# Performance work log

Hardware: AMD Instinct MI355X
Metric: run time of the kernel (lower is better)

## Reference

```python
import jax, jax.numpy as jnp
import numpy as np

# Cleaned/faithful JAX port of TATLMPLayer. The original torch code has obvious
# typos (edge_type_feature_embedding used before assignment, self.weight_mlp vs
# self._weight_mlp, missing dim= in concatenate, elementwise mult of (B,E,K) with
# (K,D)); we implement the clearly intended math: two-level masked-softmax
# message passing over an incidence matrix H, gumbel-softmax typed edge
# embeddings, and a 4-head cross-attention to polyline features.

NEG_SLOPE = 0.01  # torch leaky_relu default
TAU = 0.5         # gumbel-softmax temperature 1/2


def _mlp(x, W1, b1, W2, b2):
    return jnp.maximum(x @ W1 + b1, 0.0) @ W2 + b2


def setup_inputs() -> dict:
    B, N, E, P, D, T, K, Hd = 2, 256, 512, 256, 128, 8, 8, 256
    key = jax.random.key(0)
    ks = jax.random.split(key, 40)
    g = lambda i, shape, s=0.05: jax.random.normal(ks[i], shape, dtype=jnp.float32) * s
    return {
        "agent_features": jax.random.normal(ks[0], (B, N, D), dtype=jnp.float32),
        "agent_types": jax.random.uniform(ks[1], (B, N, T), dtype=jnp.float32),
        "polyline_features": jax.random.normal(ks[2], (B, P, D), dtype=jnp.float32),
        "H": (jax.random.uniform(ks[3], (B, E, N)) < 0.1).astype(jnp.float32),
        "type_emb": g(4, (K, D)),
        "w_W1": g(5, (2 * D, Hd)), "w_b1": g(6, (Hd,)), "w_W2": g(7, (Hd, 1)), "w_b2": g(8, (1,)),
        "d_W1": g(9, (D + T, Hd)), "d_b1": g(10, (Hd,)), "d_W2": g(11, (Hd, K)), "d_b2": g(12, (K,)),
        "f_W1": g(13, (D + T, Hd)), "f_b1": g(14, (Hd,)), "f_W2": g(15, (Hd, 1)), "f_b2": g(16, (1,)),
        "o_W1": g(17, (4 * D, Hd)), "o_b1": g(18, (Hd,)), "o_W2": g(19, (Hd, D)), "o_b2": g(20, (D,)),
        "q_W": g(21, (3 * D, D)), "q_b": g(22, (D,)),
        "k_W": g(23, (D, D)), "k_b": g(24, (D,)),
        "v_W": g(25, (D, D)), "v_b": g(26, (D,)),
        "iq_W": g(27, (D, D)), "iq_b": g(28, (D,)),
        "ik_W": g(29, (D, D)), "ik_b": g(30, (D,)),
        "iv_W": g(31, (D, D)), "iv_b": g(32, (D,)),
        "op_W": g(33, (D, D)), "op_b": g(34, (D,)),
    }


def reference(agent_features, agent_types, polyline_features, H, type_emb,
              w_W1, w_b1, w_W2, w_b2, d_W1, d_b1, d_W2, d_b2,
              f_W1, f_b1, f_W2, f_b2, o_W1, o_b1, o_W2, o_b2,
              q_W, q_b, k_W, k_b, v_W, v_b,
              iq_W, iq_b, ik_W, ik_b, iv_W, iv_b, op_W, op_b):
    B, N, D = agent_features.shape
    E = H.shape[1]

    # level 1: incidence-aggregated edge features
    ef_init = jnp.einsum('ben,bnd->bed', H, agent_features)            # (B,E,D)
    pair = jnp.concatenate([
        jnp.broadcast_to(ef_init[:, :, None, :], (B, E, N, D)),
        jnp.broadcast_to(agent_features[:, None, :, :], (B, E, N, D))], axis=-1)
    ew = _mlp(pair, w_W1, w_b1, w_W2, w_b2)[..., 0]                    # (B,E,N)
    Hw = jax.nn.softmax(ew * H, axis=2) * H
    edge_features = jnp.einsum('ben,bnd->bed', Hw, agent_features)     # (B,E,D)

    # typed edge embedding via gumbel-softmax over edge types
    edge_type = jnp.einsum('ben,bnt->bet', H, agent_types)             # (B,E,T)
    et = jnp.concatenate([edge_features, edge_type], axis=-1)          # (B,E,D+T)
    logits = _mlp(et, d_W1, d_b1, d_W2, d_b2)                          # (B,E,K)
    u = jax.random.uniform(jax.random.key(42), logits.shape, minval=1e-6, maxval=1.0 - 1e-6)
    gumbel = -jnp.log(-jnp.log(u))
    distribution = jax.nn.softmax((logits + gumbel) / TAU, axis=-1)
    factor = jax.nn.sigmoid(_mlp(et, f_W1, f_b1, f_W2, f_b2))          # (B,E,1)
    edge_type_embedding = jnp.einsum('bek,kd->bed', factor * distribution, type_emb)

    # level 2: masked edge->agent message passing
    pair2 = jnp.concatenate([
        jnp.broadcast_to(edge_type_embedding[:, :, None, :], (B, E, N, D)),
        jnp.broadcast_to(agent_features[:, None, :, :], (B, E, N, D))], axis=-1)
    pair2 = pair2 * H[..., None]
    hw2 = jnp.where(_mlp(pair2, w_W1, w_b1, w_W2, w_b2)[..., 0] > 0,
                    _mlp(pair2, w_W1, w_b1, w_W2, w_b2)[..., 0], 0.0)
    # leaky relu (single-eval form)
    raw2 = _mlp(pair2, w_W1, w_b1, w_W2, w_b2)[..., 0]
    hw2 = jnp.where(raw2 > 0, raw2, NEG_SLOPE * raw2)                  # (B,E,N)
    Hw2 = jax.nn.softmax(hw2, axis=2) * H
    msg = jnp.einsum('ben,bef->bnf', Hw2,
                     jnp.concatenate([edge_features, edge_type_embedding], axis=-1))
    agent_feat = jnp.concatenate([msg, agent_features], axis=-1)       # (B,N,3D)

    # cross-attention to polylines (4 heads)
    Q = agent_feat @ q_W + q_b
    Kp = polyline_features @ k_W + k_b
    Vp = polyline_features @ v_W + v_b
    q2 = Q @ iq_W + iq_b
    k2 = Kp @ ik_W + ik_b
    v2 = Vp @ iv_W + iv_b
    nh, hd = 4, D // 4
    qh = q2.reshape(B, N, nh, hd)
    kh = k2.reshape(B, -1, nh, hd)
    vh = v2.reshape(B, -1, nh, hd)
    att = jax.nn.softmax(jnp.einsum('bqhd,bkhd->bhqk', qh, kh) / jnp.sqrt(jnp.float32(hd)), axis=-1)
    o = jnp.einsum('bhqk,bkhd->bqhd', att, vh).reshape(B, N, D)
    polyline_new = o @ op_W + op_b                                     # (B,N,D)

    agent_new = _mlp(jnp.concatenate([agent_feat, polyline_new], axis=-1),
                     o_W1, o_b1, o_W2, o_b2)                           # (B,N,D)
    return agent_new, polyline_new
```

## Files before the change

kernel.cpp:

```cpp
#include <hip/hip_runtime.h>
#include <math.h>

#define BB 2
#define NN 256
#define EE 512
#define PP 256
#define DD 128
#define TT 8
#define KK 8
#define HDIM 256

#define WS_G      0
#define WS_C0     8192
#define WS_EF0    8256
#define WS_ETYPE  139328
#define WS_V      147520
#define WS_EDGEF  278592
#define WS_ETE    409664
#define WS_HWT    540736
#define WS_AGF    802880
#define WS_Q2     999488
#define WS_K2     1065024
#define WS_V2     1130560

#define GB_INC  16
#define GB_V    1040
#define GB_KV   1168
#define GB_END  1296

__device__ inline unsigned rotl32(unsigned x, int d){ return (x<<d)|(x>>(32-d)); }

__device__ inline float bits_to_gumbel(unsigned bits){
  float f = __uint_as_float((bits>>9)|0x3f800000u) - 1.0f;
  const float minv = 1e-6f;
  const float maxv = 1.0f - 1e-6f;
  float u = f*(maxv-minv) + minv;
  u = fmaxf(minv, u);
  return -logf(-logf(u));
}

__device__ __forceinline__ void f4fma(float4& a, float x, const float4& w){
  a.x += x*w.x; a.y += x*w.y; a.z += x*w.z; a.w += x*w.w;
}
// ... 74 lines not shown
  #pragma unroll
  for (int r=0;r<4;r++) *(float4*)&part[(ks*4+r)*DD+c]=a[r];
  __syncthreads();
  int cc=t&127, rh=t>>7;
  for (int rr=rh; rr<4; rr+=2){
    float s=0.f;
    #pragma unroll
    for (int k2=0;k2<8;k2++) s+=part[(k2*4+rr)*DD+cc];
    dst[(size_t)(r0+rr)*DD+cc]=s+bias[cc];
  }
  __syncthreads();
}

__global__ void prep_kernel(float* g, float* c0, const float* w_b1,
                            const float* w_W2, const float* w_b2,
                            const float* Hm, const float* af, const float* at,
                            float* ef0, float* etype,
                            const float* wW1, float* Vout,
                            const float* pf,
                            const float* kW, const float* kb, const float* ikW, const float* ikb,
                            const float* vW, const float* vb, const float* ivW, const float* ivb,
                            float* k2, float* v2){
  __shared__ int   ecomp[NN];
  __shared__ int   wcnt[4];
  __shared__ float accl[2][DD];
  __shared__ float acctl[2][TT];
  __shared__ float xs[4][DD];
  __shared__ float part[4*4*HDIM];
  __shared__ float wred[16];
  __shared__ float bufB[4][DD];
  int blk = blockIdx.x;
  int t = threadIdx.x;
  int lane = t & 63, wid = t >> 6;

  if (blk < GB_INC){
    int j = blk*256 + t;
    {
      const unsigned k0=0u, k1=42u;
      const unsigned ks2 = k0^k1^0x1BD11BDAu;
      unsigned x0 = (unsigned)j, x1 = (unsigned)j + 4096u;
      const int r0[4]={13,15,26,6}, r1[4]={17,29,16,24};
      x0 += k0; x1 += k1;
      #pragma unroll
      for(int i=0;i<4;i++){ x0+=x1; x1=rotl32(x1,r0[i]); x1^=x0; }
      x0+=k1; x1+=ks2+1u;
      #pragma unroll
      for(int i=0;i<4;i++){ x0+=x1; x1=rotl32(x1,r1[i]); x1^=x0; }
      x0+=ks2; x1+=k0+2u;
      #pragma unroll
      for(int i=0;i<4;i++){ x0+=x1; x1=rotl32(x1,r0[i]); x1^=x0; }
      x0+=k0; x1+=k1+3u;
      #pragma unroll
      for(int i=0;i<4;i++){ x0+=x1; x1=rotl32(x1,r1[i]); x1^=x0; }
      x0+=k1; x1+=ks2+4u;
      #pragma unroll
      for(int i=0;i<4;i++){ x0+=x1; x1=rotl32(x1,r0[i]); x1^=x0; }
      x0+=ks2; x1+=k0+5u;
      g[j]      = bits_to_gumbel(x0);
      g[j+4096] = bits_to_gumbel(x1);
    }
    if (blk == 0){
      float v4[4];
      v4[0] = fmaxf(w_b1[t],0.f)*w_W2[t]; v4[1]=0.f; v4[2]=0.f; v4[3]=0.f;
      block_reduce4_sum(v4, wred);
      if (t==0) c0[0] = v4[0] + w_b2[0];
    }
  } else if (blk < GB_V){
    int be = blk - GB_INC;
    int b  = be >> 9;
    const float* Hrow = Hm + (size_t)be*NN;
    int n = t;
    bool pred = (Hrow[n] != 0.f);
    unsigned long long mask = __ballot(pred);
    if (lane==0) wcnt[wid] = __popcll(mask);
    int off = __popcll(mask & ((1ull<<lane)-1ull));
    __syncthreads();
    int wb = 0;
    for (int ww=0; ww<wid; ww++) wb += wcnt[ww];
    if (pred) ecomp[wb+off] = n;
    int total = wcnt[0]+wcnt[1]+wcnt[2]+wcnt[3];
    __syncthreads();
    int d = t & 127, h2 = t >> 7;
    float acc = 0.f, acct = 0.f;
    for (int i=h2; i<total; i+=2){
      int n2 = ecomp[i];
      acc += af[((size_t)b*NN+n2)*DD + d];
      if (d < TT) acct += at[((size_t)b*NN+n2)*TT + d];
    }
    accl[h2][d] = acc;
    if (d < TT) acctl[h2][d] = acct;
    __syncthreads();
    if (t < DD) ef0[(size_t)be*DD + t] = accl[0][t] + accl[1][t];
    if (t < TT) etype[(size_t)be*TT + t] = acctl[0][t] + acctl[1][t];
  } else if (blk < GB_KV){
    int r0 = (blk - GB_V)*4;
    const float* W = wW1 + (size_t)DD*HDIM;
    for (int i=t;i<4*DD;i+=256) xs[i>>7][i&127] = af[(size_t)(r0+(i>>7))*DD + (i&127)];
    __syncthreads();
    int c = (t&63)*4, ks = t>>6;
    float4 acc[4];
    #pragma unroll
    for (int r=0;r<4;r++) acc[r]=make_float4(0.f,0.f,0.f,0.f);
    #pragma unroll 8
    for (int i=ks*32; i<ks*32+32; i++){
      float4 w = *(const float4*)&W[(size_t)i*HDIM + c];
      #pragma unroll
      for (int r=0;r<4;r++) f4fma(acc[r], xs[r][i], w);
    }
    #pragma unroll
    for (int r=0;r<4;r++) *(float4*)&part[(ks*4+r)*HDIM + c] = acc[r];
    __syncthreads();
    #pragma unroll
    for (int r=0;r<4;r++){
      float s = (part[(0*4+r)*HDIM+t] + part[(1*4+r)*HDIM+t])
              + (part[(2*4+r)*HDIM+t] + part[(3*4+r)*HDIM+t]);
      Vout[(size_t)(r0+r)*HDIM + t] = s;
    }
  } else {
    int r0 = (blk - GB_KV)*4;
    for (int i=t;i<4*DD;i+=256) xs[i>>7][i&127] = pf[(size_t)(r0+(i>>7))*DD + (i&127)];
    __syncthreads();
    mlp128_lds (xs, kW, kb, bufB, part, t);
    mlp128_glob(bufB, ikW, ikb, k2, r0, part, t);
    mlp128_lds (xs, vW, vb, bufB, part, t);
    mlp128_glob(bufB, ivW, ivb, v2, r0, part, t);
  }
}

__global__ void l1_fused_kernel(const float* ef0, const float* Vm, const float* Hm,
                                const float* af, const float* wW1, const float* wb1,
                                const float* wW2, const float* wb2, float* edgef){
  __shared__ float xs[4][DD];
  __shared__ float part[4*4*HDIM];
  __shared__ float u[4][HDIM];
  __shared__ float w2l[HDIM];
  __shared__ float hwls[4][NN];
  __shared__ float wred[16];
  __shared__ int   ncomp[4][NN];
  __shared__ float ncw[4][NN];
  __shared__ int   ncnt[4];
  int e0 = blockIdx.x*4;
  int b  = e0 >> 9;
  int t  = threadIdx.x;
  int lane = t & 63, wid = t >> 6;

  for (int i=t;i<4*DD;i+=256) xs[i>>7][i&127] = ef0[(size_t)(e0+(i>>7))*DD + (i&127)];
  w2l[t] = wW2[t];
  __syncthreads();
  {
    int c = (t&63)*4, ks = t>>6;
    float4 acc[4];
    #pragma unroll
    for (int r=0;r<4;r++) acc[r]=make_float4(0.f,0.f,0.f,0.f);
    #pragma unroll 8
    for (int i=ks*32; i<ks*32+32; i++){
      float4 w = *(const float4*)&wW1[(size_t)i*HDIM + c];
      #pragma unroll
      for (int r=0;r<4;r++) f4fma(acc[r], xs[r][i], w);
    }
    #pragma unroll
    for (int r=0;r<4;r++) *(float4*)&part[(ks*4+r)*HDIM + c] = acc[r];
  }
  __syncthreads();
  {
    float bv = wb1[t];
    #pragma unroll
    for (int r=0;r<4;r++){
      float s = (part[(0*4+r)*HDIM+t] + part[(1*4+r)*HDIM+t])
              + (part[(2*4+r)*HDIM+t] + part[(3*4+r)*HDIM+t]);
      u[r][t] = s + bv;
    }
  }
  __syncthreads();
  int n = t;
  const float4* Vrow = (const float4*)(Vm + ((size_t)(b*NN)+n)*HDIM);
  float acc[4]={0.f,0.f,0.f,0.f};
  #pragma unroll 4
  for (int ii=0;ii<HDIM/4;ii++){
    float4 v = Vrow[ii];
    float w0=w2l[4*ii+0], w1=w2l[4*ii+1], wc=w2l[4*ii+2], w3=w2l[4*ii+3];
    #pragma unroll
    for (int r=0;r<4;r++){
      acc[r] += fmaxf(u[r][4*ii+0]+v.x,0.f)*w0
              + fmaxf(u[r][4*ii+1]+v.y,0.f)*w1
              + fmaxf(u[r][4*ii+2]+v.z,0.f)*wc
              + fmaxf(u[r][4*ii+3]+v.w,0.f)*w3;
    }
  }
  float b2v = wb2[0];
  float x[4], hv[4];
  #pragma unroll
  for (int r=0;r<4;r++){
    hv[r] = Hm[(size_t)(e0+r)*NN + n];
    x[r] = (hv[r]!=0.f) ? (acc[r]+b2v) : 0.f;
  }
  float m4[4]={x[0],x[1],x[2],x[3]};
  block_reduce4_max(m4, wred);
  float p4[4];
  #pragma unroll
  for (int r=0;r<4;r++) p4[r]=expf(x[r]-m4[r]);
  float s4[4]={p4[0],p4[1],p4[2],p4[3]};
  block_reduce4_sum(s4, wred);
  #pragma unroll
  for (int r=0;r<4;r++)
    hwls[r][n] = (hv[r]!=0.f) ? p4[r]/s4[r] : 0.f;
  __syncthreads();
  {
    int r = wid;
    int base = 0;
    #pragma unroll
    for (int c4=0;c4<4;c4++){
      int n2 = c4*64 + lane;
      float w = hwls[r][n2];
      bool pred = (w != 0.f);
      unsigned long long mask = __ballot(pred);
      int off = __popcll(mask & ((1ull<<lane)-1ull));
      if (pred){ ncomp[r][base+off] = n2; ncw[r][base+off] = w; }
      base += __popcll(mask);
    }
    if (lane==0) ncnt[r] = base;
  }
  __syncthreads();
  {
    int d = t & 127, eh = t >> 7;
    #pragma unroll
    for (int rr=0;rr<2;rr++){
      int r = eh*2 + rr;
      int tot = ncnt[r];
      float a = 0.f;
      for (int i=0;i<tot;i++)
        a += ncw[r][i]*af[((size_t)b*NN+ncomp[r][i])*DD + d];
      edgef[(size_t)(e0+r)*DD + d] = a;
    }
  }
}

__global__ void l2_fused_kernel(const float* edgef, const float* etype, const float* g,
                                const float* dW1, const float* db1, const float* dW2, const float* db2,
                                const float* fW1, const float* fb1, const float* fW2, const float* fb2,
                                const float* type_emb,
                                const float* wW1, const float* wb1, const float* wW2, const float* wb2,
                                const float* c0p, const float* Hm, const float* Vm,
                                float* ete_g, float* HwT){
  __shared__ float et4[4][DD+TT+8];
  __shared__ float partD[4*4*HDIM];
  __shared__ float partF[4*4*HDIM];
  __shared__ float hd4[4][HDIM];
  __shared__ float w2s[HDIM*KK];
  __shared__ float redsm[256];
  __shared__ float wred[16];
  __shared__ float facs[4];
  __shared__ float zz[4][KK];
  __shared__ float pzs[4][KK];
  __shared__ float fdv[4][KK];
  int e0 = blockIdx.x*4;
  int b  = e0 >> 9;
  int t  = threadIdx.x;
  const int KW = DD+TT;

  for (int i=t;i<4*KW;i+=256){
    int r=i/KW, cc=i%KW;
    et4[r][cc] = (cc<DD) ? edgef[(size_t)(e0+r)*DD+cc] : etype[(size_t)(e0+r)*TT + (cc-DD)];
  }
  for (int i=t;i<HDIM*KK;i+=256) w2s[i] = dW2[i];
  __syncthreads();
  int c=(t&63)*4, ks=t>>6;
  {
    float4 ad4[4], af4[4];
    #pragma unroll
    for (int r=0;r<4;r++){ ad4[r]=make_float4(0.f,0.f,0.f,0.f); af4[r]=make_float4(0.f,0.f,0.f,0.f); }
    #pragma unroll 4
    for (int i=ks*34;i<ks*34+34;i++){
      float4 wd = *(const float4*)&dW1[(size_t)i*HDIM+c];
      float4 wf = *(const float4*)&fW1[(size_t)i*HDIM+c];
      #pragma unroll
      for (int r=0;r<4;r++){ float x=et4[r][i]; f4fma(ad4[r],x,wd); f4fma(af4[r],x,wf); }
    }
    #pragma unroll
    for (int r=0;r<4;r++){
      *(float4*)&partD[(ks*4+r)*HDIM+c]=ad4[r];
      *(float4*)&partF[(ks*4+r)*HDIM+c]=af4[r];
    }
  }
  __syncthreads();
  {
    float bd = db1[t];
    float bf = fb1[t], fw = fW2[t];
    float v4[4];
    #pragma unroll
    for (int r=0;r<4;r++){
      float sd = (partD[(0*4+r)*HDIM+t]+partD[(1*4+r)*HDIM+t])
               + (partD[(2*4+r)*HDIM+t]+partD[(3*4+r)*HDIM+t]);
      hd4[r][t] = fmaxf(sd+bd, 0.f);
      float sf = (partF[(0*4+r)*HDIM+t]+partF[(1*4+r)*HDIM+t])
               + (partF[(2*4+r)*HDIM+t]+partF[(3*4+r)*HDIM+t]);
      v4[r] = fmaxf(sf+bf,0.f)*fw;
    }
    block_reduce4_sum(v4, wred);
    if (t<4) facs[t] = 1.f/(1.f+expf(-(v4[t]+fb2[0])));
  }
  {
    int rr_ = t>>6, kk_ = (t>>3)&7, jj_ = t&7;
    float lp = 0.f;
    #pragma unroll 4
    for (int i=0;i<32;i++){
      int h = jj_ + 8*i;
      lp += hd4[rr_][h]*w2s[h*KK + kk_];
    }
    redsm[t] = lp;
  }
// ... 21 lines not shown
    for (int k2=0;k2<KK;k2++) s += pzs[r][k2];
    fdv[r][k] = facs[r]*pzs[r][k]/s;
  }
  __syncthreads();
  {
    int d = t&127;
    #pragma unroll
    for (int rr=0;rr<2;rr++){
      int r = 2*rr + (t>>7);
      float a = 0.f;
      #pragma unroll
      for (int k=0;k<KK;k++) a += fdv[r][k]*type_emb[(size_t)k*DD + d];
      et4[r][d] = a;
      ete_g[(size_t)(e0+r)*DD + d] = a;
    }
    w2s[t] = wW2[t];
  }
  __syncthreads();
  {
    float4 a[4];
    #pragma unroll
    for (int r=0;r<4;r++) a[r]=make_float4(0.f,0.f,0.f,0.f);
    #pragma unroll 8
    for (int i=ks*32;i<ks*32+32;i++){
      float4 w = *(const float4*)&wW1[(size_t)i*HDIM+c];
      #pragma unroll
      for (int r=0;r<4;r++) f4fma(a[r], et4[r][i], w);
    }
    #pragma unroll
    for (int r=0;r<4;r++) *(float4*)&partD[(ks*4+r)*HDIM+c]=a[r];
  }
  __syncthreads();
  {
    float bv = wb1[t];
    #pragma unroll
    for (int r=0;r<4;r++){
      float s = (partD[(0*4+r)*HDIM+t]+partD[(1*4+r)*HDIM+t])
              + (partD[(2*4+r)*HDIM+t]+partD[(3*4+r)*HDIM+t]);
      hd4[r][t] = s + bv;
    }
  }
  __syncthreads();
  {
    int n = t;
    const float4* Vrow = (const float4*)(Vm + ((size_t)(b*NN)+n)*HDIM);
    float acc[4]={0.f,0.f,0.f,0.f};
    #pragma unroll 4
    for (int ii=0;ii<HDIM/4;ii++){
      float4 v = Vrow[ii];
      float w0=w2s[4*ii+0], w1=w2s[4*ii+1], wc=w2s[4*ii+2], w3=w2s[4*ii+3];
      #pragma unroll
      for (int r=0;r<4;r++){
        acc[r] += fmaxf(hd4[r][4*ii+0]+v.x,0.f)*w0
                + fmaxf(hd4[r][4*ii+1]+v.y,0.f)*w1
                + fmaxf(hd4[r][4*ii+2]+v.z,0.f)*wc
                + fmaxf(hd4[r][4*ii+3]+v.w,0.f)*w3;
      }
    }
    float b2v = wb2[0];
    float c0 = c0p[0];
    float x[4], hv[4];
    #pragma unroll
    for (int r=0;r<4;r++){
      hv[r] = Hm[(size_t)(e0+r)*NN + n];
      float raw = (hv[r]!=0.f) ? (acc[r]+b2v) : c0;
// ... 4 lines not shown
    float p4[4];
    #pragma unroll
    for (int r=0;r<4;r++) p4[r]=expf(x[r]-m4[r]);
    float s4[4]={p4[0],p4[1],p4[2],p4[3]};
    block_reduce4_sum(s4, wred);
    int eb = e0 & 511;
    float4 o4;
    o4.x = (hv[0]!=0.f)? p4[0]/s4[0] : 0.f;
    o4.y = (hv[1]!=0.f)? p4[1]/s4[1] : 0.f;
    o4.z = (hv[2]!=0.f)? p4[2]/s4[2] : 0.f;
    o4.w = (hv[3]!=0.f)? p4[3]/s4[3] : 0.f;
    *(float4*)(HwT + ((size_t)(b*NN)+n)*EE + eb) = o4;
  }
}

__global__ void msgq2_kernel(const float* HwT, const float* edgef, const float* ete,
                             const float* af, const float* qW, const float* qb,
                             const float* iqW, const float* iqb,
                             float* agf, float* q2){
  __shared__ int   ecomp[EE];
  __shared__ float wcomp[EE];
  __shared__ int   wcnt[4];
  __shared__ float agfl[3*DD];
  __shared__ float part[8*DD];
  __shared__ float Qs[DD];
  int bn = blockIdx.x; int b = bn>>8; int f = threadIdx.x;
  int lane = f & 63, wid = f >> 6;
  const float* wrow = HwT + (size_t)bn*EE;
  int total = 0;
  #pragma unroll
  for (int p=0;p<2;p++){
    int e = p*256 + f;
    float w = wrow[e];
    bool pred = (w != 0.f);
    unsigned long long mask = __ballot(pred);
    if (lane==0) wcnt[wid] = __popcll(mask);
    int off = __popcll(mask & ((1ull<<lane)-1ull));
    __syncthreads();
    int wb = total;
    for (int ww=0; ww<wid; ww++) wb += wcnt[ww];
    if (pred){ ecomp[wb+off] = e; wcomp[wb+off] = w; }
    total += wcnt[0]+wcnt[1]+wcnt[2]+wcnt[3];
    __syncthreads();
  }
  float acc = 0.f;
  const float* srcbase = (f < DD) ? (edgef + (size_t)b*EE*DD + f)
                                  : (ete   + (size_t)b*EE*DD + (f-DD));
  for (int i=0;i<total;i++){
    acc += wcomp[i] * srcbase[(size_t)ecomp[i]*DD];
  }
  agfl[f] = acc;
  agf[(size_t)bn*(3*DD)+f] = acc;
  if (f < DD){
    float av = af[(size_t)bn*DD + f];
    agfl[2*DD+f] = av;
    agf[(size_t)bn*(3*DD) + 2*DD + f] = av;
  }
  __syncthreads();
  int c=(f&31)*4, ks=f>>5;
  {
    float4 a = make_float4(0.f,0.f,0.f,0.f);
    #pragma unroll 4
    for (int i=ks*48;i<ks*48+48;i++){
      float4 w = *(const float4*)&qW[(size_t)i*DD+c];
      f4fma(a, agfl[i], w);
    }
    *(float4*)&part[ks*DD+c]=a;
  }
  __syncthreads();
  if (f<DD){
    float s=0.f;
    #pragma unroll
    for (int k=0;k<8;k++) s+=part[k*DD+f];
    Qs[f]=s+qb[f];
  }
  __syncthreads();
  {
    float4 a = make_float4(0.f,0.f,0.f,0.f);
    #pragma unroll 4
    for (int i=ks*16;i<ks*16+16;i++){
      float4 w = *(const float4*)&iqW[(size_t)i*DD+c];
      f4fma(a, Qs[i], w);
    }
    *(float4*)&part[ks*DD+c]=a;
  }
  __syncthreads();
  if (f<DD){
    float s=0.f;
    #pragma unroll
    for (int k=0;k<8;k++) s+=part[k*DD+f];
    q2[(size_t)bn*DD+f]=s+iqb[f];
  }
}

__global__ void attnfinal_kernel(const float* q2, const float* k2, const float* v2,
                                 const float* op_W, const float* op_b,
                                 const float* agf,
                                 const float* oW1, const float* ob1,
                                 const float* oW2, const float* ob2,
                                 float* pnew, float* anew){
  __shared__ float qr[2][DD];
  __shared__ float att[2][4][PP+1];
  __shared__ float o_l[2][DD];
  __shared__ float part[8*2*DD];
  __shared__ float pnl[2][DD];
  __shared__ float xs[2][4*DD];
  __shared__ float hid[2][HDIM];
  int r0 = blockIdx.x*2; int b = r0 >> 8; int t = threadIdx.x;
  for (int i=t;i<2*DD;i+=256) qr[i>>7][i&127] = q2[(size_t)(r0+(i>>7))*DD + (i&127)];
  __syncthreads();
  const float scale = 0.17677669529663687f;
  const float* krow = k2 + ((size_t)(b*PP) + t)*DD;
  #pragma unroll
  for (int h=0;h<4;h++){
    const float4* k4 = (const float4*)(krow + h*32);
    float s[2]={0.f,0.f};
    #pragma unroll
    for (int jj=0;jj<8;jj++){
      float4 kk = k4[jj];
      #pragma unroll
      for (int r=0;r<2;r++){
        s[r] += qr[r][h*32+jj*4+0]*kk.x + qr[r][h*32+jj*4+1]*kk.y
              + qr[r][h*32+jj*4+2]*kk.z + qr[r][h*32+jj*4+3]*kk.w;
      }
    }
    #pragma unroll
    for (int r=0;r<2;r++) att[r][h][t] = s[r]*scale;
  }
  __syncthreads();
  {
    int lane = t & 63, wid = t >> 6;
    for (int q = wid; q < 8; q += 4){
      int r = q >> 2, h = q & 3;
      float v0 = att[r][h][lane],     v1 = att[r][h][lane+64],
            ve = att[r][h][lane+128], v3 = att[r][h][lane+192];
      float m = fmaxf(fmaxf(v0,v1), fmaxf(ve,v3));
      #pragma unroll
      for (int s2=32;s2>0;s2>>=1) m = fmaxf(m, __shfl_xor(m, s2, 64));
      float e0 = expf(v0-m), e1 = expf(v1-m), e2 = expf(ve-m), e3 = expf(v3-m);
      float ss = (e0+e1)+(e2+e3);
      #pragma unroll
      for (int s2=32;s2>0;s2>>=1) ss += __shfl_xor(ss, s2, 64);
      float inv = 1.f/ss;
      att[r][h][lane] = e0*inv; att[r][h][lane+64] = e1*inv;
      att[r][h][lane+128] = e2*inv; att[r][h][lane+192] = e3*inv;
    }
  }
  __syncthreads();
  int c=(t&31)*4, ps=t>>5; int h2 = c>>5;
  {
    float4 acc[2];
    #pragma unroll
    for (int r=0;r<2;r++) acc[r]=make_float4(0.f,0.f,0.f,0.f);
    #pragma unroll 4
    for (int i=0;i<32;i++){
      int p = ps*32+i;
      float4 v = *(const float4*)&v2[((size_t)(b*PP)+p)*DD + c];
      #pragma unroll
      for (int r=0;r<2;r++) f4fma(acc[r], att[r][h2][p], v);
    }
    #pragma unroll
    for (int r=0;r<2;r++) *(float4*)&part[(ps*2+r)*DD+c]=acc[r];
  }
  __syncthreads();
  {
    int cc=t&127, r=t>>7;
    float s=0.f;
    #pragma unroll
    for (int k2_=0;k2_<8;k2_++) s+=part[(k2_*2+r)*DD+cc];
    o_l[r][cc]=s;
  }
  __syncthreads();
  {
    float4 a2[2];
    #pragma unroll
    for (int r=0;r<2;r++) a2[r]=make_float4(0.f,0.f,0.f,0.f);
    #pragma unroll 4
    for (int i=ps*16;i<ps*16+16;i++){
      float4 w = *(const float4*)&op_W[(size_t)i*DD + c];
      #pragma unroll
      for (int r=0;r<2;r++) f4fma(a2[r], o_l[r][i], w);
    }
    #pragma unroll
    for (int r=0;r<2;r++) *(float4*)&part[(ps*2+r)*DD+c]=a2[r];
  }
  __syncthreads();
  {
    int cc=t&127, r=t>>7;
    float s=0.f;
    #pragma unroll
    for (int k2_=0;k2_<8;k2_++) s+=part[(k2_*2+r)*DD+cc];
    float pv = s+op_b[cc];
    pnl[r][cc] = pv;
    pnew[(size_t)(r0+r)*DD+cc] = pv;
  }
  for (int i=t;i<2*(3*DD);i+=256){
    int r = i/(3*DD), cc = i%(3*DD);
    xs[r][cc] = agf[(size_t)(r0+r)*(3*DD)+cc];
  }
  __syncthreads();
  if (t < 2*DD){
    int r = t>>7, cc = t&127;
    xs[r][3*DD+cc] = pnl[r][cc];
  }
  __syncthreads();
  {
    int c1=(t&63)*4, ks1=t>>6;
    float4 acc[2];
    #pragma unroll
    for (int r=0;r<2;r++) acc[r]=make_float4(0.f,0.f,0.f,0.f);
    #pragma unroll 8
    for (int i=ks1*128;i<ks1*128+128;i++){
      float4 w = *(const float4*)&oW1[(size_t)i*HDIM+c1];
      #pragma unroll
      for (int r=0;r<2;r++) f4fma(acc[r], xs[r][i], w);
    }
    #pragma unroll
    for (int r=0;r<2;r++) *(float4*)&part[(ks1*2+r)*HDIM+c1]=acc[r];
  }
  __syncthreads();
  {
    float bv = ob1[t];
    #pragma unroll
    for (int r=0;r<2;r++){
      float s = (part[(0*2+r)*HDIM+t]+part[(1*2+r)*HDIM+t])
              + (part[(2*2+r)*HDIM+t]+part[(3*2+r)*HDIM+t]);
      hid[r][t] = fmaxf(s+bv, 0.f);
    }
  }
  __syncthreads();
// ... 3 lines not shown
    for (int r=0;r<2;r++) a2[r]=make_float4(0.f,0.f,0.f,0.f);
    #pragma unroll 8
    for (int h=ps*32;h<ps*32+32;h++){
      float4 w = *(const float4*)&oW2[(size_t)h*DD+c];
      #pragma unroll
      for (int r=0;r<2;r++) f4fma(a2[r], hid[r][h], w);
    }
    #pragma unroll
    for (int r=0;r<2;r++) *(float4*)&part[(ps*2+r)*DD+c]=a2[r];
  }
  __syncthreads();
  {
    int cc=t&127, r=t>>7;
    float s=0.f;
    #pragma unroll
    for (int k2_=0;k2_<8;k2_++) s+=part[(k2_*2+r)*DD+cc];
    anew[(size_t)(r0+r)*DD+cc]=s+ob2[cc];
  }
}

extern "C" void kernel_launch(void* const* d_in, const int* in_sizes, int n_in,
                              void* d_out, int out_size, void* d_ws, size_t ws_size,
                              hipStream_t stream) {
  const float* af       = (const float*)d_in[0];
  const float* at       = (const float*)d_in[1];
  const float* pf       = (const float*)d_in[2];
  const float* Hm       = (const float*)d_in[3];
  const float* type_emb = (const float*)d_in[4];
  const float* w_W1 = (const float*)d_in[5];
  const float* w_b1 = (const float*)d_in[6];
  const float* w_W2 = (const float*)d_in[7];
  const float* w_b2 = (const float*)d_in[8];
// ... 17 lines not shown
  const float* v_b  = (const float*)d_in[26];
  const float* iq_W = (const float*)d_in[27];
  const float* iq_b = (const float*)d_in[28];
  const float* ik_W = (const float*)d_in[29];
  const float* ik_b = (const float*)d_in[30];
  const float* iv_W = (const float*)d_in[31];
  const float* iv_b = (const float*)d_in[32];
  const float* op_W = (const float*)d_in[33];
  const float* op_b = (const float*)d_in[34];

  float* ws   = (float*)d_ws;
  float* out  = (float*)d_out;
  float* anew = out;
  float* pnew = out + BB*NN*DD;

  prep_kernel<<<GB_END, 256, 0, stream>>>(
      ws+WS_G, ws+WS_C0, w_b1, w_W2, w_b2,
      Hm, af, at, ws+WS_EF0, ws+WS_ETYPE, w_W1, ws+WS_V,
      pf, k_W,k_b,ik_W,ik_b, v_W,v_b,iv_W,iv_b,
      ws+WS_K2, ws+WS_V2);
  l1_fused_kernel<<<256,256,0,stream>>>(
      ws+WS_EF0, ws+WS_V, Hm, af, w_W1, w_b1, w_W2, w_b2, ws+WS_EDGEF);
  l2_fused_kernel<<<256,256,0,stream>>>(
      ws+WS_EDGEF, ws+WS_ETYPE, ws+WS_G,
      d_W1,d_b1,d_W2,d_b2, f_W1,f_b1,f_W2,f_b2, type_emb,
      w_W1, w_b1, w_W2, w_b2, ws+WS_C0, Hm, ws+WS_V,
      ws+WS_ETE, ws+WS_HWT);
  msgq2_kernel<<<BB*NN,256,0,stream>>>(
      ws+WS_HWT, ws+WS_EDGEF, ws+WS_ETE, af,
      q_W, q_b, iq_W, iq_b, ws+WS_AGF, ws+WS_Q2);
  attnfinal_kernel<<<256,256,0,stream>>>(
      ws+WS_Q2, ws+WS_K2, ws+WS_V2, op_W, op_b,
      ws+WS_AGF, o_W1,o_b1,o_W2,o_b2, pnew, anew);
}
```

Measured before the change: 91.78 us.

## Fuse edge stages into one kernel and merge message/Q with attention kernel

The incidence-gather that produced ef0/etype moves out of the prep kernel and into a single edge kernel, which now also runs the level-1 softmax and the level-2 typed-edge stage, so ef0, etype and the intermediate edge features no longer round-trip through global memory. The message aggregation and Q projection are merged into the attention/output kernel, which processes two agents per block and drops the agf and q2 workspace buffers. This cuts five launches to three and removes several global writes and reads. In exchange, the fused kernels are longer and serialised, with large LDS footprints that can lower occupancy. The agent kernel runs only 256 blocks, each doing the per-agent gather twice in sequence.

Result: no change. 93.58 us (+2.0%).

```diff
diff --git a/kernel.cpp b/kernel.cpp
--- a/kernel.cpp
+++ b/kernel.cpp
@@ -12,21 +12,16 @@
 
 #define WS_G      0
 #define WS_C0     8192
-#define WS_EF0    8256
-#define WS_ETYPE  139328
-#define WS_V      147520
-#define WS_EDGEF  278592
-#define WS_ETE    409664
-#define WS_HWT    540736
-#define WS_AGF    802880
-#define WS_Q2     999488
-#define WS_K2     1065024
-#define WS_V2     1130560
-
-#define GB_INC  16
-#define GB_V    1040
-#define GB_KV   1168
-#define GB_END  1296
+#define WS_V      8256
+#define WS_EDGEF  139328
+#define WS_ETE    270400
+#define WS_HWT    401472
+#define WS_K2     663616
+#define WS_V2     729152
+
+#define PB_GUM 16
+#define PB_V   144
+#define PB_END 272
 
 __device__ inline unsigned rotl32(unsigned x, int d){ return (x<<d)|(x>>(32-d)); }
 
@@ -131,47 +126,40 @@
 
 __global__ void prep_kernel(float* g, float* c0, const float* w_b1,
                             const float* w_W2, const float* w_b2,
-                            const float* Hm, const float* af, const float* at,
-                            float* ef0, float* etype,
-                            const float* wW1, float* Vout,
+                            const float* af, const float* wW1, float* Vout,
                             const float* pf,
                             const float* kW, const float* kb, const float* ikW, const float* ikb,
                             const float* vW, const float* vb, const float* ivW, const float* ivb,
                             float* k2, float* v2){
-  __shared__ int   ecomp[NN];
-  __shared__ int   wcnt[4];
-  __shared__ float accl[2][DD];
-  __shared__ float acctl[2][TT];
   __shared__ float xs[4][DD];
   __shared__ float part[4*4*HDIM];
   __shared__ float wred[16];
   __shared__ float bufB[4][DD];
   int blk = blockIdx.x;
   int t = threadIdx.x;
-  int lane = t & 63, wid = t >> 6;
-
-  if (blk < GB_INC){
+
+  if (blk < PB_GUM){
     int j = blk*256 + t;
     {
       const unsigned k0=0u, k1=42u;
       const unsigned ks2 = k0^k1^0x1BD11BDAu;
       unsigned x0 = (unsigned)j, x1 = (unsigned)j + 4096u;
-      const int r0[4]={13,15,26,6}, r1[4]={17,29,16,24};
+      const int r0_[4]={13,15,26,6}, r1_[4]={17,29,16,24};
       x0 += k0; x1 += k1;
       #pragma unroll
-      for(int i=0;i<4;i++){ x0+=x1; x1=rotl32(x1,r0[i]); x1^=x0; }
+      for(int i=0;i<4;i++){ x0+=x1; x1=rotl32(x1,r0_[i]); x1^=x0; }
       x0+=k1; x1+=ks2+1u;
       #pragma unroll
-      for(int i=0;i<4;i++){ x0+=x1; x1=rotl32(x1,r1[i]); x1^=x0; }
+      for(int i=0;i<4;i++){ x0+=x1; x1=rotl32(x1,r1_[i]); x1^=x0; }
       x0+=ks2; x1+=k0+2u;
       #pragma unroll
-      for(int i=0;i<4;i++){ x0+=x1; x1=rotl32(x1,r0[i]); x1^=x0; }
+      for(int i=0;i<4;i++){ x0+=x1; x1=rotl32(x1,r0_[i]); x1^=x0; }
       x0+=k0; x1+=k1+3u;
       #pragma unroll
-      for(int i=0;i<4;i++){ x0+=x1; x1=rotl32(x1,r1[i]); x1^=x0; }
+      for(int i=0;i<4;i++){ x0+=x1; x1=rotl32(x1,r1_[i]); x1^=x0; }
       x0+=k1; x1+=ks2+4u;
       #pragma unroll
-      for(int i=0;i<4;i++){ x0+=x1; x1=rotl32(x1,r0[i]); x1^=x0; }
+      for(int i=0;i<4;i++){ x0+=x1; x1=rotl32(x1,r0_[i]); x1^=x0; }
       x0+=ks2; x1+=k0+5u;
       g[j]      = bits_to_gumbel(x0);
       g[j+4096] = bits_to_gumbel(x1);
@@ -182,35 +170,8 @@
       block_reduce4_sum(v4, wred);
       if (t==0) c0[0] = v4[0] + w_b2[0];
     }
-  } else if (blk < GB_V){
-    int be = blk - GB_INC;
-    int b  = be >> 9;
-    const float* Hrow = Hm + (size_t)be*NN;
-    int n = t;
-    bool pred = (Hrow[n] != 0.f);
-    unsigned long long mask = __ballot(pred);
-    if (lane==0) wcnt[wid] = __popcll(mask);
-    int off = __popcll(mask & ((1ull<<lane)-1ull));
-    __syncthreads();
-    int wb = 0;
-    for (int ww=0; ww<wid; ww++) wb += wcnt[ww];
-    if (pred) ecomp[wb+off] = n;
-    int total = wcnt[0]+wcnt[1]+wcnt[2]+wcnt[3];
-    __syncthreads();
-    int d = t & 127, h2 = t >> 7;
-    float acc = 0.f, acct = 0.f;
-    for (int i=h2; i<total; i+=2){
-      int n2 = ecomp[i];
-      acc += af[((size_t)b*NN+n2)*DD + d];
-      if (d < TT) acct += at[((size_t)b*NN+n2)*TT + d];
-    }
-    accl[h2][d] = acc;
-    if (d < TT) acctl[h2][d] = acct;
-    __syncthreads();
-    if (t < DD) ef0[(size_t)be*DD + t] = accl[0][t] + accl[1][t];
-    if (t < TT) etype[(size_t)be*TT + t] = acctl[0][t] + acctl[1][t];
-  } else if (blk < GB_KV){
-    int r0 = (blk - GB_V)*4;
+  } else if (blk < PB_V){
+    int r0 = (blk - PB_GUM)*4;
     const float* W = wW1 + (size_t)DD*HDIM;
     for (int i=t;i<4*DD;i+=256) xs[i>>7][i&127] = af[(size_t)(r0+(i>>7))*DD + (i&127)];
     __syncthreads();
@@ -234,7 +195,7 @@
       Vout[(size_t)(r0+r)*HDIM + t] = s;
     }
   } else {
-    int r0 = (blk - GB_KV)*4;
+    int r0 = (blk - PB_V)*4;
     for (int i=t;i<4*DD;i+=256) xs[i>>7][i&127] = pf[(size_t)(r0+(i>>7))*DD + (i&127)];
     __syncthreads();
     mlp128_lds (xs, kW, kb, bufB, part, t);
@@ -244,145 +205,155 @@
   }
 }
 
-__global__ void l1_fused_kernel(const float* ef0, const float* Vm, const float* Hm,
-                                const float* af, const float* wW1, const float* wb1,
-                                const float* wW2, const float* wb2, float* edgef){
-  __shared__ float xs[4][DD];
-  __shared__ float part[4*4*HDIM];
-  __shared__ float u[4][HDIM];
+__global__ void edge_kernel(const float* Hm, const float* af, const float* at,
+                            const float* Vm,
+                            const float* wW1, const float* wb1, const float* wW2, const float* wb2,
+                            const float* dW1, const float* db1, const float* dW2, const float* db2,
+                            const float* fW1, const float* fb1, const float* fW2, const float* fb2,
+                            const float* type_emb, const float* g, const float* c0p,
+                            float* edgef_g, float* ete_g, float* HwT){
+  __shared__ float bufA[4*4*HDIM];
+  __shared__ float bufB[4*4*HDIM];
+  __shared__ float w2s[HDIM*KK];
   __shared__ float w2l[HDIM];
-  __shared__ float hwls[4][NN];
-  __shared__ float wred[16];
-  __shared__ int   ncomp[4][NN];
-  __shared__ float ncw[4][NN];
-  __shared__ int   ncnt[4];
-  int e0 = blockIdx.x*4;
-  int b  = e0 >> 9;
-  int t  = threadIdx.x;
-  int lane = t & 63, wid = t >> 6;
-
-  for (int i=t;i<4*DD;i+=256) xs[i>>7][i&127] = ef0[(size_t)(e0+(i>>7))*DD + (i&127)];
-  w2l[t] = wW2[t];
-  __syncthreads();
-  {
-    int c = (t&63)*4, ks = t>>6;
-    float4 acc[4];
-    #pragma unroll
-    for (int r=0;r<4;r++) acc[r]=make_float4(0.f,0.f,0.f,0.f);
-    #pragma unroll 8
-    for (int i=ks*32; i<ks*32+32; i++){
-      float4 w = *(const float4*)&wW1[(size_t)i*HDIM + c];
-      #pragma unroll
-      for (int r=0;r<4;r++) f4fma(acc[r], xs[r][i], w);
-    }
-    #pragma unroll
-    for (int r=0;r<4;r++) *(float4*)&part[(ks*4+r)*HDIM + c] = acc[r];
-  }
-  __syncthreads();
-  {
-    float bv = wb1[t];
-    #pragma unroll
-    for (int r=0;r<4;r++){
-      float s = (part[(0*4+r)*HDIM+t] + part[(1*4+r)*HDIM+t])
-              + (part[(2*4+r)*HDIM+t] + part[(3*4+r)*HDIM+t]);
-      u[r][t] = s + bv;
-    }
-  }
-  __syncthreads();
-  int n = t;
-  const float4* Vrow = (const float4*)(Vm + ((size_t)(b*NN)+n)*HDIM);
-  float acc[4]={0.f,0.f,0.f,0.f};
-  #pragma unroll 4
-  for (int ii=0;ii<HDIM/4;ii++){
-    float4 v = Vrow[ii];
-    float w0=w2l[4*ii+0], w1=w2l[4*ii+1], wc=w2l[4*ii+2], w3=w2l[4*ii+3];
-    #pragma unroll
-    for (int r=0;r<4;r++){
-      acc[r] += fmaxf(u[r][4*ii+0]+v.x,0.f)*w0
-              + fmaxf(u[r][4*ii+1]+v.y,0.f)*w1
-              + fmaxf(u[r][4*ii+2]+v.z,0.f)*wc
-              + fmaxf(u[r][4*ii+3]+v.w,0.f)*w3;
-    }
-  }
-  float b2v = wb2[0];
-  float x[4], hv[4];
-  #pragma unroll
-  for (int r=0;r<4;r++){
-    hv[r] = Hm[(size_t)(e0+r)*NN + n];
-    x[r] = (hv[r]!=0.f) ? (acc[r]+b2v) : 0.f;
-  }
-  float m4[4]={x[0],x[1],x[2],x[3]};
-  block_reduce4_max(m4, wred);
-  float p4[4];
-  #pragma unroll
-  for (int r=0;r<4;r++) p4[r]=expf(x[r]-m4[r]);
-  float s4[4]={p4[0],p4[1],p4[2],p4[3]};
-  block_reduce4_sum(s4, wred);
-  #pragma unroll
-  for (int r=0;r<4;r++)
-    hwls[r][n] = (hv[r]!=0.f) ? p4[r]/s4[r] : 0.f;
-  __syncthreads();
-  {
-    int r = wid;
-    int base = 0;
-    #pragma unroll
-    for (int c4=0;c4<4;c4++){
-      int n2 = c4*64 + lane;
-      float w = hwls[r][n2];
-      bool pred = (w != 0.f);
-      unsigned long long mask = __ballot(pred);
-      int off = __popcll(mask & ((1ull<<lane)-1ull));
-      if (pred){ ncomp[r][base+off] = n2; ncw[r][base+off] = w; }
-      base += __popcll(mask);
-    }
-    if (lane==0) ncnt[r] = base;
-  }
-  __syncthreads();
-  {
-    int d = t & 127, eh = t >> 7;
-    #pragma unroll
-    for (int rr=0;rr<2;rr++){
-      int r = eh*2 + rr;
-      int tot = ncnt[r];
-      float a = 0.f;
-      for (int i=0;i<tot;i++)
-        a += ncw[r][i]*af[((size_t)b*NN+ncomp[r][i])*DD + d];
-      edgef[(size_t)(e0+r)*DD + d] = a;
-    }
-  }
-}
-
-__global__ void l2_fused_kernel(const float* edgef, const float* etype, const float* g,
-                                const float* dW1, const float* db1, const float* dW2, const float* db2,
-                                const float* fW1, const float* fb1, const float* fW2, const float* fb2,
-                                const float* type_emb,
-                                const float* wW1, const float* wb1, const float* wW2, const float* wb2,
-                                const float* c0p, const float* Hm, const float* Vm,
-                                float* ete_g, float* HwT){
-  __shared__ float et4[4][DD+TT+8];
-  __shared__ float partD[4*4*HDIM];
-  __shared__ float partF[4*4*HDIM];
+  __shared__ float et4[4][144];
   __shared__ float hd4[4][HDIM];
-  __shared__ float w2s[HDIM*KK];
   __shared__ float redsm[256];
   __shared__ float wred[16];
   __shared__ float facs[4];
   __shared__ float zz[4][KK];
   __shared__ float pzs[4][KK];
   __shared__ float fdv[4][KK];
+  __shared__ int   hcnt[4];
+  float* u    = bufB;
+  float* hwls = bufB + 1024;
+  int*   hcomp= (int*)(bufB + 2048);
+
   int e0 = blockIdx.x*4;
   int b  = e0 >> 9;
   int t  = threadIdx.x;
-  const int KW = DD+TT;
-
-  for (int i=t;i<4*KW;i+=256){
-    int r=i/KW, cc=i%KW;
-    et4[r][cc] = (cc<DD) ? edgef[(size_t)(e0+r)*DD+cc] : etype[(size_t)(e0+r)*TT + (cc-DD)];
-  }
+  int lane = t & 63, wid = t >> 6;
+
+  w2l[t] = wW2[t];
   for (int i=t;i<HDIM*KK;i+=256) w2s[i] = dW2[i];
-  __syncthreads();
-  int c=(t&63)*4, ks=t>>6;
-  {
+
+  {
+    int r = wid;
+    const float* Hrow = Hm + (size_t)(e0+r)*NN;
+    int base = 0;
+    #pragma unroll
+    for (int c4=0;c4<4;c4++){
+      int n2 = c4*64 + lane;
+      bool pred = (Hrow[n2] != 0.f);
+      unsigned long long mask = __ballot(pred);
+      int off = __popcll(mask & ((1ull<<lane)-1ull));
+      if (pred) hcomp[r*256+base+off] = n2;
+      base += __popcll(mask);
+    }
+    if (lane==0) hcnt[r] = base;
+  }
+  __syncthreads();
+  {
+    int d = t & 127, eh = t >> 7;
+    #pragma unroll
+    for (int rr=0;rr<2;rr++){
+      int r = eh*2 + rr;
+      int tot = hcnt[r];
+      float a = 0.f, a2 = 0.f;
+      for (int i=0;i<tot;i++){
+        int n2 = hcomp[r*256+i];
+        a += af[((size_t)b*NN+n2)*DD + d];
+        if (d < TT) a2 += at[((size_t)b*NN+n2)*TT + d];
+      }
+      et4[r][d] = a;
+      if (d < TT) et4[r][DD+d] = a2;
+    }
+  }
+  __syncthreads();
+  {
+    int c=(t&63)*4, ks=t>>6;
+    float4 acc[4];
+    #pragma unroll
+    for (int r=0;r<4;r++) acc[r]=make_float4(0.f,0.f,0.f,0.f);
+    #pragma unroll 8
+    for (int i=ks*32; i<ks*32+32; i++){
+      float4 w = *(const float4*)&wW1[(size_t)i*HDIM + c];
+      #pragma unroll
+      for (int r=0;r<4;r++) f4fma(acc[r], et4[r][i], w);
+    }
+    #pragma unroll
+    for (int r=0;r<4;r++) *(float4*)&bufA[(ks*4+r)*HDIM + c] = acc[r];
+  }
+  __syncthreads();
+  {
+    float bv = wb1[t];
+    #pragma unroll
+    for (int r=0;r<4;r++){
+      float s = (bufA[(0*4+r)*HDIM+t] + bufA[(1*4+r)*HDIM+t])
+              + (bufA[(2*4+r)*HDIM+t] + bufA[(3*4+r)*HDIM+t]);
+      u[r*HDIM + t] = s + bv;
+    }
+  }
+  __syncthreads();
+  {
+    int n = t;
+    const float4* Vrow = (const float4*)(Vm + ((size_t)(b*NN)+n)*HDIM);
+    float acc[4]={0.f,0.f,0.f,0.f};
+    #pragma unroll 4
+    for (int ii=0;ii<HDIM/4;ii++){
+      float4 v = Vrow[ii];
+      float w0=w2l[4*ii+0], w1=w2l[4*ii+1], wc=w2l[4*ii+2], w3=w2l[4*ii+3];
+      #pragma unroll
+      for (int r=0;r<4;r++){
+        acc[r] += fmaxf(u[r*HDIM+4*ii+0]+v.x,0.f)*w0
+                + fmaxf(u[r*HDIM+4*ii+1]+v.y,0.f)*w1
+                + fmaxf(u[r*HDIM+4*ii+2]+v.z,0.f)*wc
+                + fmaxf(u[r*HDIM+4*ii+3]+v.w,0.f)*w3;
+      }
+    }
+    float b2v = wb2[0];
+    float x[4], hv[4];
+    #pragma unroll
+    for (int r=0;r<4;r++){
+      hv[r] = Hm[(size_t)(e0+r)*NN + n];
+      x[r] = (hv[r]!=0.f) ? (acc[r]+b2v) : 0.f;
+    }
+    float m4[4]={x[0],x[1],x[2],x[3]};
+    block_reduce4_max(m4, wred);
+    float p4[4];
+    #pragma unroll
+    for (int r=0;r<4;r++) p4[r]=expf(x[r]-m4[r]);
+    float s4[4]={p4[0],p4[1],p4[2],p4[3]};
+    block_reduce4_sum(s4, wred);
+    #pragma unroll
+    for (int r=0;r<4;r++)
+      hwls[r*NN+n] = (hv[r]!=0.f) ? p4[r]/s4[r] : 0.f;
+  }
+  __syncthreads();
+  {
+    int d = t & 127, eh = t >> 7;
+    float eg[2];
+    #pragma unroll
+    for (int rr=0;rr<2;rr++){
+      int r = eh*2 + rr;
+      int tot = hcnt[r];
+      float a = 0.f;
+      for (int i=0;i<tot;i++){
+        int n2 = hcomp[r*256+i];
+        a += hwls[r*NN+n2]*af[((size_t)b*NN+n2)*DD + d];
+      }
+      eg[rr] = a;
+    }
+    #pragma unroll
+    for (int rr=0;rr<2;rr++){
+      int r = eh*2 + rr;
+      et4[r][d] = eg[rr];
+      edgef_g[(size_t)(e0+r)*DD + d] = eg[rr];
+    }
+  }
+  __syncthreads();
+  {
+    int c=(t&63)*4, ks=t>>6;
     float4 ad4[4], af4[4];
     #pragma unroll
     for (int r=0;r<4;r++){ ad4[r]=make_float4(0.f,0.f,0.f,0.f); af4[r]=make_float4(0.f,0.f,0.f,0.f); }
@@ -395,8 +366,8 @@
     }
     #pragma unroll
     for (int r=0;r<4;r++){
-      *(float4*)&partD[(ks*4+r)*HDIM+c]=ad4[r];
-      *(float4*)&partF[(ks*4+r)*HDIM+c]=af4[r];
+      *(float4*)&bufA[(ks*4+r)*HDIM+c]=ad4[r];
+      *(float4*)&bufB[(ks*4+r)*HDIM+c]=af4[r];
     }
   }
   __syncthreads();
@@ -406,11 +377,11 @@
     float v4[4];
     #pragma unroll
     for (int r=0;r<4;r++){
-      float sd = (partD[(0*4+r)*HDIM+t]+partD[(1*4+r)*HDIM+t])
-               + (partD[(2*4+r)*HDIM+t]+partD[(3*4+r)*HDIM+t]);
+      float sd = (bufA[(0*4+r)*HDIM+t]+bufA[(1*4+r)*HDIM+t])
+               + (bufA[(2*4+r)*HDIM+t]+bufA[(3*4+r)*HDIM+t]);
       hd4[r][t] = fmaxf(sd+bd, 0.f);
-      float sf = (partF[(0*4+r)*HDIM+t]+partF[(1*4+r)*HDIM+t])
-               + (partF[(2*4+r)*HDIM+t]+partF[(3*4+r)*HDIM+t]);
+      float sf = (bufB[(0*4+r)*HDIM+t]+bufB[(1*4+r)*HDIM+t])
+               + (bufB[(2*4+r)*HDIM+t]+bufB[(3*4+r)*HDIM+t]);
       v4[r] = fmaxf(sf+bf,0.f)*fw;
     }
     block_reduce4_sum(v4, wred);
@@ -462,10 +433,10 @@
       et4[r][d] = a;
       ete_g[(size_t)(e0+r)*DD + d] = a;
     }
-    w2s[t] = wW2[t];
-  }
-  __syncthreads();
-  {
+  }
+  __syncthreads();
+  {
+    int c=(t&63)*4, ks=t>>6;
     float4 a[4];
     #pragma unroll
     for (int r=0;r<4;r++) a[r]=make_float4(0.f,0.f,0.f,0.f);
@@ -476,15 +447,15 @@
       for (int r=0;r<4;r++) f4fma(a[r], et4[r][i], w);
     }
     #pragma unroll
-    for (int r=0;r<4;r++) *(float4*)&partD[(ks*4+r)*HDIM+c]=a[r];
+    for (int r=0;r<4;r++) *(float4*)&bufA[(ks*4+r)*HDIM+c]=a[r];
   }
   __syncthreads();
   {
     float bv = wb1[t];
     #pragma unroll
     for (int r=0;r<4;r++){
-      float s = (partD[(0*4+r)*HDIM+t]+partD[(1*4+r)*HDIM+t])
-              + (partD[(2*4+r)*HDIM+t]+partD[(3*4+r)*HDIM+t]);
+      float s = (bufA[(0*4+r)*HDIM+t]+bufA[(1*4+r)*HDIM+t])
+              + (bufA[(2*4+r)*HDIM+t]+bufA[(3*4+r)*HDIM+t]);
       hd4[r][t] = s + bv;
     }
   }
@@ -496,7 +467,7 @@
     #pragma unroll 4
     for (int ii=0;ii<HDIM/4;ii++){
       float4 v = Vrow[ii];
-      float w0=w2s[4*ii+0], w1=w2s[4*ii+1], wc=w2s[4*ii+2], w3=w2s[4*ii+3];
+      float w0=w2l[4*ii+0], w1=w2l[4*ii+1], wc=w2l[4*ii+2], w3=w2l[4*ii+3];
       #pragma unroll
       for (int r=0;r<4;r++){
         acc[r] += fmaxf(hd4[r][4*ii+0]+v.x,0.f)*w0
@@ -531,100 +502,100 @@
   }
 }
 
-__global__ void msgq2_kernel(const float* HwT, const float* edgef, const float* ete,
-                             const float* af, const float* qW, const float* qb,
-                             const float* iqW, const float* iqb,
-                             float* agf, float* q2){
+__global__ void agent_kernel(const float* HwT, const float* edgef, const float* ete,
+                             const float* af,
+                             const float* qW, const float* qb, const float* iqW, const float* iqb,
+                             const float* k2, const float* v2,
+                             const float* op_W, const float* op_b,
+                             const float* oW1, const float* ob1,
+                             const float* oW2, const float* ob2,
+                             float* pnew, float* anew){
   __shared__ int   ecomp[EE];
   __shared__ float wcomp[EE];
   __shared__ int   wcnt[4];
-  __shared__ float agfl[3*DD];
-  __shared__ float part[8*DD];
-  __shared__ float Qs[DD];
-  int bn = blockIdx.x; int b = bn>>8; int f = threadIdx.x;
-  int lane = f & 63, wid = f >> 6;
-  const float* wrow = HwT + (size_t)bn*EE;
-  int total = 0;
-  #pragma unroll
-  for (int p=0;p<2;p++){
-    int e = p*256 + f;
-    float w = wrow[e];
-    bool pred = (w != 0.f);
-    unsigned long long mask = __ballot(pred);
-    if (lane==0) wcnt[wid] = __popcll(mask);
-    int off = __popcll(mask & ((1ull<<lane)-1ull));
-    __syncthreads();
-    int wb = total;
-    for (int ww=0; ww<wid; ww++) wb += wcnt[ww];
-    if (pred){ ecomp[wb+off] = e; wcomp[wb+off] = w; }
-    total += wcnt[0]+wcnt[1]+wcnt[2]+wcnt[3];
-    __syncthreads();
-  }
-  float acc = 0.f;
-  const float* srcbase = (f < DD) ? (edgef + (size_t)b*EE*DD + f)
-                                  : (ete   + (size_t)b*EE*DD + (f-DD));
-  for (int i=0;i<total;i++){
-    acc += wcomp[i] * srcbase[(size_t)ecomp[i]*DD];
-  }
-  agfl[f] = acc;
-  agf[(size_t)bn*(3*DD)+f] = acc;
-  if (f < DD){
-    float av = af[(size_t)bn*DD + f];
-    agfl[2*DD+f] = av;
-    agf[(size_t)bn*(3*DD) + 2*DD + f] = av;
-  }
-  __syncthreads();
-  int c=(f&31)*4, ks=f>>5;
-  {
-    float4 a = make_float4(0.f,0.f,0.f,0.f);
-    #pragma unroll 4
-    for (int i=ks*48;i<ks*48+48;i++){
-      float4 w = *(const float4*)&qW[(size_t)i*DD+c];
-      f4fma(a, agfl[i], w);
-    }
-    *(float4*)&part[ks*DD+c]=a;
-  }
-  __syncthreads();
-  if (f<DD){
-    float s=0.f;
-    #pragma unroll
-    for (int k=0;k<8;k++) s+=part[k*DD+f];
-    Qs[f]=s+qb[f];
-  }
-  __syncthreads();
-  {
-    float4 a = make_float4(0.f,0.f,0.f,0.f);
-    #pragma unroll 4
-    for (int i=ks*16;i<ks*16+16;i++){
-      float4 w = *(const float4*)&iqW[(size_t)i*DD+c];
-      f4fma(a, Qs[i], w);
-    }
-    *(float4*)&part[ks*DD+c]=a;
-  }
-  __syncthreads();
-  if (f<DD){
-    float s=0.f;
-    #pragma unroll
-    for (int k=0;k<8;k++) s+=part[k*DD+f];
-    q2[(size_t)bn*DD+f]=s+iqb[f];
-  }
-}
-
-__global__ void attnfinal_kernel(const float* q2, const float* k2, const float* v2,
-                                 const float* op_W, const float* op_b,
-                                 const float* agf,
-                                 const float* oW1, const float* ob1,
-                                 const float* oW2, const float* ob2,
-                                 float* pnew, float* anew){
+  __shared__ float agfl[2][512];
+  __shared__ float part[2048];
+  __shared__ float Qs[2][DD];
   __shared__ float qr[2][DD];
   __shared__ float att[2][4][PP+1];
   __shared__ float o_l[2][DD];
-  __shared__ float part[8*2*DD];
-  __shared__ float pnl[2][DD];
-  __shared__ float xs[2][4*DD];
   __shared__ float hid[2][HDIM];
-  int r0 = blockIdx.x*2; int b = r0 >> 8; int t = threadIdx.x;
-  for (int i=t;i<2*DD;i+=256) qr[i>>7][i&127] = q2[(size_t)(r0+(i>>7))*DD + (i&127)];
+  int n0 = blockIdx.x*2; int b = n0 >> 8; int t = threadIdx.x;
+  int lane = t & 63, wid = t >> 6;
+
+  for (int rr=0;rr<2;rr++){
+    int bn = n0 + rr;
+    const float* wrow = HwT + (size_t)bn*EE;
+    int total = 0;
+    #pragma unroll
+    for (int p=0;p<2;p++){
+      int e = p*256 + t;
+      float w = wrow[e];
+      bool pred = (w != 0.f);
+      unsigned long long mask = __ballot(pred);
+      if (lane==0) wcnt[wid] = __popcll(mask);
+      int off = __popcll(mask & ((1ull<<lane)-1ull));
+      __syncthreads();
+      int wb = total;
+      for (int ww=0; ww<wid; ww++) wb += wcnt[ww];
+      if (pred){ ecomp[wb+off] = e; wcomp[wb+off] = w; }
+      total += wcnt[0]+wcnt[1]+wcnt[2]+wcnt[3];
+      __syncthreads();
+    }
+    float acc = 0.f;
+    const float* srcbase = (t < DD) ? (edgef + (size_t)b*EE*DD + t)
+                                    : (ete   + (size_t)b*EE*DD + (t-DD));
+    for (int i=0;i<total;i++){
+      acc += wcomp[i] * srcbase[(size_t)ecomp[i]*DD];
+    }
+    agfl[rr][t] = acc;
+    if (t < DD) agfl[rr][2*DD+t] = af[(size_t)bn*DD + t];
+    __syncthreads();
+  }
+  int c=(t&31)*4, ps=t>>5;
+  {
+    float4 a[2];
+    #pragma unroll
+    for (int r=0;r<2;r++) a[r]=make_float4(0.f,0.f,0.f,0.f);
+    #pragma unroll 4
+    for (int i=ps*48;i<ps*48+48;i++){
+      float4 w = *(const float4*)&qW[(size_t)i*DD+c];
+      #pragma unroll
+      for (int r=0;r<2;r++) f4fma(a[r], agfl[r][i], w);
+    }
+    #pragma unroll
+    for (int r=0;r<2;r++) *(float4*)&part[(ps*2+r)*DD+c]=a[r];
+  }
+  __syncthreads();
+  {
+    int cc=t&127, r=t>>7;
+    float s=0.f;
+    #pragma unroll
+    for (int k=0;k<8;k++) s+=part[(k*2+r)*DD+cc];
+    Qs[r][cc]=s+qb[cc];
+  }
+  __syncthreads();
+  {
+    float4 a[2];
+    #pragma unroll
+    for (int r=0;r<2;r++) a[r]=make_float4(0.f,0.f,0.f,0.f);
+    #pragma unroll 4
+    for (int i=ps*16;i<ps*16+16;i++){
+      float4 w = *(const float4*)&iqW[(size_t)i*DD+c];
+      #pragma unroll
+      for (int r=0;r<2;r++) f4fma(a[r], Qs[r][i], w);
+    }
+    #pragma unroll
+    for (int r=0;r<2;r++) *(float4*)&part[(ps*2+r)*DD+c]=a[r];
+  }
+  __syncthreads();
+  {
+    int cc=t&127, r=t>>7;
+    float s=0.f;
+    #pragma unroll
+    for (int k=0;k<8;k++) s+=part[(k*2+r)*DD+cc];
+    qr[r][cc]=s+iqb[cc];
+  }
   __syncthreads();
   const float scale = 0.17677669529663687f;
   const float* krow = k2 + ((size_t)(b*PP) + t)*DD;
@@ -646,7 +617,6 @@
   }
   __syncthreads();
   {
-    int lane = t & 63, wid = t >> 6;
     for (int q = wid; q < 8; q += 4){
       int r = q >> 2, h = q & 3;
       float v0 = att[r][h][lane],     v1 = att[r][h][lane+64],
@@ -664,7 +634,7 @@
     }
   }
   __syncthreads();
-  int c=(t&31)*4, ps=t>>5; int h2 = c>>5;
+  int h2 = c >> 5;
   {
     float4 acc[2];
     #pragma unroll
@@ -684,7 +654,7 @@
     int cc=t&127, r=t>>7;
     float s=0.f;
     #pragma unroll
-    for (int k2_=0;k2_<8;k2_++) s+=part[(k2_*2+r)*DD+cc];
+    for (int k=0;k<8;k++) s+=part[(k*2+r)*DD+cc];
     o_l[r][cc]=s;
   }
   __syncthreads();
@@ -706,19 +676,10 @@
     int cc=t&127, r=t>>7;
     float s=0.f;
     #pragma unroll
-    for (int k2_=0;k2_<8;k2_++) s+=part[(k2_*2+r)*DD+cc];
+    for (int k=0;k<8;k++) s+=part[(k*2+r)*DD+cc];
     float pv = s+op_b[cc];
-    pnl[r][cc] = pv;
-    pnew[(size_t)(r0+r)*DD+cc] = pv;
-  }
-  for (int i=t;i<2*(3*DD);i+=256){
-    int r = i/(3*DD), cc = i%(3*DD);
-    xs[r][cc] = agf[(size_t)(r0+r)*(3*DD)+cc];
-  }
-  __syncthreads();
-  if (t < 2*DD){
-    int r = t>>7, cc = t&127;
-    xs[r][3*DD+cc] = pnl[r][cc];
+    agfl[r][3*DD+cc] = pv;
+    pnew[(size_t)(n0+r)*DD+cc] = pv;
   }
   __syncthreads();
   {
@@ -730,7 +691,7 @@
     for (int i=ks1*128;i<ks1*128+128;i++){
       float4 w = *(const float4*)&oW1[(size_t)i*HDIM+c1];
       #pragma unroll
-      for (int r=0;r<2;r++) f4fma(acc[r], xs[r][i], w);
+      for (int r=0;r<2;r++) f4fma(acc[r], agfl[r][i], w);
     }
     #pragma unroll
     for (int r=0;r<2;r++) *(float4*)&part[(ks1*2+r)*HDIM+c1]=acc[r];
@@ -764,8 +725,8 @@
     int cc=t&127, r=t>>7;
     float s=0.f;
     #pragma unroll
-    for (int k2_=0;k2_<8;k2_++) s+=part[(k2_*2+r)*DD+cc];
-    anew[(size_t)(r0+r)*DD+cc]=s+ob2[cc];
+    for (int k=0;k<8;k++) s+=part[(k*2+r)*DD+cc];
+    anew[(size_t)(n0+r)*DD+cc]=s+ob2[cc];
   }
 }
 
@@ -813,22 +774,20 @@
   float* anew = out;
   float* pnew = out + BB*NN*DD;
 
-  prep_kernel<<<GB_END, 256, 0, stream>>>(
+  prep_kernel<<<PB_END, 256, 0, stream>>>(
       ws+WS_G, ws+WS_C0, w_b1, w_W2, w_b2,
-      Hm, af, at, ws+WS_EF0, ws+WS_ETYPE, w_W1, ws+WS_V,
+      af, w_W1, ws+WS_V,
       pf, k_W,k_b,ik_W,ik_b, v_W,v_b,iv_W,iv_b,
       ws+WS_K2, ws+WS_V2);
-  l1_fused_kernel<<<256,256,0,stream>>>(
-      ws+WS_EF0, ws+WS_V, Hm, af, w_W1, w_b1, w_W2, w_b2, ws+WS_EDGEF);
-  l2_fused_kernel<<<256,256,0,stream>>>(
-      ws+WS_EDGEF, ws+WS_ETYPE, ws+WS_G,
-      d_W1,d_b1,d_W2,d_b2, f_W1,f_b1,f_W2,f_b2, type_emb,
-      w_W1, w_b1, w_W2, w_b2, ws+WS_C0, Hm, ws+WS_V,
-      ws+WS_ETE, ws+WS_HWT);
-  msgq2_kernel<<<BB*NN,256,0,stream>>>(
+  edge_kernel<<<256,256,0,stream>>>(
+      Hm, af, at, ws+WS_V,
+      w_W1, w_b1, w_W2, w_b2,
+      d_W1,d_b1,d_W2,d_b2, f_W1,f_b1,f_W2,f_b2,
+      type_emb, ws+WS_G, ws+WS_C0,
+      ws+WS_EDGEF, ws+WS_ETE, ws+WS_HWT);
+  agent_kernel<<<256,256,0,stream>>>(
       ws+WS_HWT, ws+WS_EDGEF, ws+WS_ETE, af,
-      q_W, q_b, iq_W, iq_b, ws+WS_AGF, ws+WS_Q2);
-  attnfinal_kernel<<<256,256,0,stream>>>(
-      ws+WS_Q2, ws+WS_K2, ws+WS_V2, op_W, op_b,
-      ws+WS_AGF, o_W1,o_b1,o_W2,o_b2, pnew, anew);
-}
+      q_W, q_b, iq_W, iq_b,
+      ws+WS_K2, ws+WS_V2, op_W, op_b,
+      o_W1,o_b1,o_W2,o_b2, pnew, anew);
+}
```
